# Kernel optimization log

Hardware: AMD Instinct MI355X
Metric: run time of the kernel (lower is better)

## Reference

```python
import jax, jax.numpy as jnp
import numpy as np

B, S, D_IN, D_OUT = 4, 4096, 512, 512


def setup_inputs() -> dict:
    key = jax.random.key(0)
    k1, k2, k3, k4 = jax.random.split(key, 4)
    sc = 1.0 / np.sqrt(D_IN)
    return {
        "x": jax.random.normal(k1, (B, S, D_IN), dtype=jnp.float32),
        "Wq": jax.random.normal(k2, (D_OUT, D_IN), dtype=jnp.float32) * sc,
        "Wk": jax.random.normal(k3, (D_OUT, D_IN), dtype=jnp.float32) * sc,
        "Wv": jax.random.normal(k4, (D_OUT, D_IN), dtype=jnp.float32) * sc,
    }


def reference(x, Wq, Wk, Wv):
    # nn.Linear: y = x @ W.T  (no bias)
    q = jnp.einsum("bsd,ed->bse", x, Wq)  # [B,S,D_OUT]
    k = jnp.einsum("bsd,ed->bse", x, Wk)
    v = jnp.einsum("bsd,ed->bse", x, Wv)
    scale = 1.0 / jnp.sqrt(jnp.asarray(k.shape[-1], dtype=x.dtype))
    scores = jnp.einsum("bqe,bke->bqk", q, k) * scale  # [B,S,S]
    # causal mask: position q attends to k <= q
    s = x.shape[1]
    causal = jnp.tril(jnp.ones((s, s), dtype=bool))
    scores = jnp.where(causal[None, :, :], scores, -jnp.inf)
    attn = jax.nn.softmax(scores, axis=-1)
    # dropout p=0.0 -> identity
    return jnp.einsum("bqk,bke->bqe", attn, v)  # [B,S,D_OUT]
```

## Files before the change

### kernel.cpp

```cpp
#include <hip/hip_runtime.h>

typedef __attribute__((ext_vector_type(8))) short short8;
typedef __attribute__((ext_vector_type(4))) float f32x4;

#define GLD_AS1 const __attribute__((address_space(1))) void*
#define GLD_AS3 __attribute__((address_space(3))) void*

__device__ __forceinline__ unsigned short f2bf(float f) {
  unsigned u = __builtin_bit_cast(unsigned, f);
  u += 0x7fffu + ((u >> 16) & 1u);
  return (unsigned short)(u >> 16);
}
__device__ __forceinline__ float bf2f(unsigned short h) {
  return __builtin_bit_cast(float, (unsigned)h << 16);
}

__global__ void cvt_f32_bf16(const float* __restrict__ in, unsigned short* __restrict__ out, int n4) {
  int i = blockIdx.x * blockDim.x + threadIdx.x;
  const int st = gridDim.x * blockDim.x;
  for (; i < n4; i += st) {
    float4 f = reinterpret_cast<const float4*>(in)[i];
    unsigned long long p = (unsigned long long)f2bf(f.x)
        | ((unsigned long long)f2bf(f.y) << 16)
        | ((unsigned long long)f2bf(f.z) << 32)
        | ((unsigned long long)f2bf(f.w) << 48);
    reinterpret_cast<unsigned long long*>(out)[i] = p;
  }
}

__global__ __launch_bounds__(256) void qkv_gemm(
    const unsigned short* __restrict__ xb, const unsigned short* __restrict__ wcat,
    unsigned short* __restrict__ qb, unsigned short* __restrict__ kb,
    unsigned short* __restrict__ vtb) {
  __shared__ unsigned short As[128 * 64];
  __shared__ unsigned short Bs[128 * 64];
  const int tid = threadIdx.x, lane = tid & 63, w = tid >> 6;
  const int m0 = blockIdx.x * 128, n0 = blockIdx.y * 128;
  const int wr = w >> 1, wc = w & 1;

  f32x4 acc[4][4];
  const f32x4 z4 = {0.f, 0.f, 0.f, 0.f};
  #pragma unroll
  for (int a = 0; a < 4; ++a)
    #pragma unroll
    for (int c = 0; c < 4; ++c) acc[a][c] = z4;

  for (int it = 0; it < 8; ++it) {
    const int k0 = it * 64;
    #pragma unroll
    for (int c = 0; c < 4; ++c) {
      const int rbase = 32 * w + 8 * c;
      const int r = rbase + (lane >> 3);
      const int c16 = (lane & 7) ^ (r & 7);
      const unsigned short* ga = xb + (size_t)(m0 + r) * 512 + k0 + c16 * 8;
      const unsigned short* gb = wcat + (size_t)(n0 + r) * 512 + k0 + c16 * 8;
      __builtin_amdgcn_global_load_lds((GLD_AS1)ga, (GLD_AS3)&As[rbase * 64], 16, 0, 0);
      __builtin_amdgcn_global_load_lds((GLD_AS1)gb, (GLD_AS3)&Bs[rbase * 64], 16, 0, 0);
    }
    __syncthreads();
    #pragma unroll
    for (int ks = 0; ks < 2; ++ks) {
      const int ck = ks * 4 + (lane >> 4);
      short8 av[4], bv[4];
      #pragma unroll
      for (int fr = 0; fr < 4; ++fr) {
        const int rl = 64 * wr + 16 * fr + (lane & 15);
        av[fr] = *reinterpret_cast<const short8*>(&As[rl * 64 + ((ck ^ (rl & 7)) << 3)]);
      }
      #pragma unroll
      for (int fc = 0; fc < 4; ++fc) {
        const int rl = 64 * wc + 16 * fc + (lane & 15);
        bv[fc] = *reinterpret_cast<const short8*>(&Bs[rl * 64 + ((ck ^ (rl & 7)) << 3)]);
      }
      #pragma unroll
      for (int fr = 0; fr < 4; ++fr)
        #pragma unroll
        for (int fc = 0; fc < 4; ++fc)
          acc[fr][fc] = __builtin_amdgcn_mfma_f32_16x16x32_bf16(av[fr], bv[fc], acc[fr][fc], 0, 0, 0);
    }
    __syncthreads();
  }

  const int which = n0 >> 9;
  #pragma unroll
  for (int fr = 0; fr < 4; ++fr) {
    #pragma unroll
    for (int fc = 0; fc < 4; ++fc) {
      const int n = n0 + 64 * wc + 16 * fc + (lane & 15);
      const int nl = n & 511;
      #pragma unroll
      for (int j = 0; j < 4; ++j) {
        const int m = m0 + 64 * wr + 16 * fr + (lane >> 4) * 4 + j;
        const unsigned short v = f2bf(acc[fr][fc][j]);
        if (which == 0)      qb[(size_t)m * 512 + nl] = v;
        else if (which == 1) kb[(size_t)m * 512 + nl] = v;
        else                 vtb[((size_t)((m >> 12) * 512 + nl)) * 4096 + (m & 4095)] = v;
      }
    }
  }
}

__global__ __launch_bounds__(512) void attn_fwd(
    const unsigned short* __restrict__ qg, const unsigned short* __restrict__ kg,
    const unsigned short* __restrict__ vtg,
    float* __restrict__ out0,
    unsigned short* __restrict__ out1,
    float* __restrict__ ml) {
  __shared__ unsigned short Ks[2][64 * 512];
  __shared__ float S_lds[64][66];
  __shared__ unsigned short P_lds[64][72];
  __shared__ float row_f[64];

  const int tid = threadIdx.x, lane = tid & 63, w = tid >> 6;
  const int idx = blockIdx.x;
  const int qt = 63 - (idx >> 3);
  const int b = (idx >> 1) & 3;
  const int half = idx & 1;
  const int nkt = qt + 1;
  const int kt0 = half ? (nkt >> 1) : 0;
  const int kt1 = half ? nkt : (nkt >> 1);
  const int q0 = qt * 64;

  const unsigned short* Qb  = qg  + (size_t)b * 4096 * 512;
  const unsigned short* Kb  = kg  + (size_t)b * 4096 * 512;
  const unsigned short* Vtb = vtg + (size_t)b * 512 * 4096;

  const int wr = w & 3, wc = w >> 2;
  const int dw = w * 64;
  const int srow = 8 * w + (lane >> 3);
  const float scale = 0.044194173824159216f;

  short8 qreg[16];
  {
    const unsigned short* qrow = Qb + (size_t)(q0 + 16 * wr + (lane & 15)) * 512 + (lane >> 4) * 8;
    #pragma unroll
    for (int ks = 0; ks < 16; ++ks)
      qreg[ks] = *reinterpret_cast<const short8*>(qrow + ks * 32);
  }

  const f32x4 z4 = {0.f, 0.f, 0.f, 0.f};
  f32x4 oacc[4][4];
  #pragma unroll
  for (int fr = 0; fr < 4; ++fr)
    #pragma unroll
    for (int fc = 0; fc < 4; ++fc) oacc[fr][fc] = z4;

  float m_run = -1e30f, l_run = 0.f;

  if (kt0 < kt1) {
    #pragma unroll
    for (int r8 = 0; r8 < 8; ++r8) {
      const int r = r8 * 8 + w;
      const unsigned short* g = Kb + (size_t)(kt0 * 64 + r) * 512 + (lane ^ (r & 7)) * 8;
      __builtin_amdgcn_global_load_lds((GLD_AS1)g, (GLD_AS3)&Ks[0][r * 512], 16, 0, 0);
    }
  }
  __syncthreads();

  int cur = 0;
  for (int kt = kt0; kt < kt1; ++kt, cur ^= 1) {
    const int kv0 = kt * 64;

    short8 vreg[2][4];
    #pragma unroll
    for (int ks = 0; ks < 2; ++ks)
      #pragma unroll
      for (int fc = 0; fc < 4; ++fc)
        vreg[ks][fc] = *reinterpret_cast<const short8*>(
            Vtb + (size_t)(dw + 16 * fc + (lane & 15)) * 4096 + kv0 + ks * 32 + (lane >> 4) * 8);

    if (kt + 1 < kt1) {
      #pragma unroll
      for (int r8 = 0; r8 < 8; ++r8) {
        const int r = r8 * 8 + w;
        const unsigned short* g = Kb + (size_t)((kt + 1) * 64 + r) * 512 + (lane ^ (r & 7)) * 8;
        __builtin_amdgcn_global_load_lds((GLD_AS1)g, (GLD_AS3)&Ks[cur ^ 1][r * 512], 16, 0, 0);
      }
    }

    f32x4 sacc[2] = {z4, z4};
    #pragma unroll
    for (int ks = 0; ks < 16; ++ks) {
      const int ck = ks * 4 + (lane >> 4);
      #pragma unroll
      for (int fc = 0; fc < 2; ++fc) {
        const int rl = 32 * wc + 16 * fc + (lane & 15);
        const short8 bv = *reinterpret_cast<const short8*>(&Ks[cur][rl * 512 + ((ck ^ (rl & 7)) << 3)]);
        sacc[fc] = __builtin_amdgcn_mfma_f32_16x16x32_bf16(qreg[ks], bv, sacc[fc], 0, 0, 0);
      }
    }
    #pragma unroll
    for (int fc = 0; fc < 2; ++fc)
      #pragma unroll
      for (int j = 0; j < 4; ++j)
        S_lds[16 * wr + (lane >> 4) * 4 + j][32 * wc + 16 * fc + (lane & 15)] = sacc[fc][j];
    __syncthreads();

    {
      const int c0 = (lane & 7) * 8;
      float v[8];
      #pragma unroll
      for (int i = 0; i < 8; ++i) {
        float s = S_lds[srow][c0 + i] * scale;
        if (kt == qt && (c0 + i) > srow) s = -1e30f;
        v[i] = s;
      }
      float pmax = v[0];
      #pragma unroll
      for (int i = 1; i < 8; ++i) pmax = fmaxf(pmax, v[i]);
      pmax = fmaxf(pmax, __shfl_xor(pmax, 1));
      pmax = fmaxf(pmax, __shfl_xor(pmax, 2));
      pmax = fmaxf(pmax, __shfl_xor(pmax, 4));
      const float m_new = fmaxf(m_run, pmax);
      const float r = __expf(m_run - m_new);
      float psum = 0.f;
      short8 pk;
      #pragma unroll
      for (int i = 0; i < 8; ++i) {
        const float p = __expf(v[i] - m_new);
        psum += p;
        pk[i] = (short)f2bf(p);
      }
      psum += __shfl_xor(psum, 1);
      psum += __shfl_xor(psum, 2);
      psum += __shfl_xor(psum, 4);
      l_run = l_run * r + psum;
      m_run = m_new;
      if ((lane & 7) == 0) row_f[srow] = r;
      *reinterpret_cast<short8*>(&P_lds[srow][c0]) = pk;
    }
    __syncthreads();

    #pragma unroll
    for (int fr = 0; fr < 4; ++fr)
      #pragma unroll
      for (int j = 0; j < 4; ++j) {
        const float f = row_f[16 * fr + (lane >> 4) * 4 + j];
        #pragma unroll
        for (int fc = 0; fc < 4; ++fc) oacc[fr][fc][j] *= f;
      }
    #pragma unroll
    for (int ks = 0; ks < 2; ++ks) {
      short8 av[4];
      #pragma unroll
      for (int fr = 0; fr < 4; ++fr)
        av[fr] = *reinterpret_cast<const short8*>(&P_lds[16 * fr + (lane & 15)][ks * 32 + (lane >> 4) * 8]);
      #pragma unroll
      for (int fr = 0; fr < 4; ++fr)
        #pragma unroll
        for (int fc = 0; fc < 4; ++fc)
          oacc[fr][fc] = __builtin_amdgcn_mfma_f32_16x16x32_bf16(av[fr], vreg[ks][fc], oacc[fr][fc], 0, 0, 0);
    }
  }

  if ((lane & 7) == 0) {
    const int rg = b * 4096 + q0 + srow;
    ml[(half * 2) * 16384 + rg]     = m_run;
    ml[(half * 2 + 1) * 16384 + rg] = l_run;
  }
  if (half == 0) {
    float* ob = out0 + (size_t)b * 4096 * 512;
    #pragma unroll
    for (int fr = 0; fr < 4; ++fr)
      #pragma unroll
      for (int j = 0; j < 4; ++j) {
        const int row = 16 * fr + (lane >> 4) * 4 + j;
        #pragma unroll
        for (int fc = 0; fc < 4; ++fc)
          ob[(size_t)(q0 + row) * 512 + dw + 16 * fc + (lane & 15)] = oacc[fr][fc][j];
      }
  } else {
    unsigned short* ob = out1 + (size_t)b * 4096 * 512;
    #pragma unroll
    for (int fr = 0; fr < 4; ++fr)
      #pragma unroll
      for (int j = 0; j < 4; ++j) {
        const int row = 16 * fr + (lane >> 4) * 4 + j;
        #pragma unroll
        for (int fc = 0; fc < 4; ++fc)
          ob[(size_t)(q0 + row) * 512 + dw + 16 * fc + (lane & 15)] = f2bf(oacc[fr][fc][j]);
      }
  }
}

__global__ void attn_merge(float* __restrict__ out, const unsigned short* __restrict__ o1,
                           const float* __restrict__ ml) {
  const int total = 16384 * 128;
  int i = blockIdx.x * blockDim.x + threadIdx.x;
  const int st = gridDim.x * blockDim.x;
  for (; i < total; i += st) {
    const int r = i >> 7;
    const float m0 = ml[r], l0 = ml[16384 + r];
    const float m1 = ml[2 * 16384 + r], l1 = ml[3 * 16384 + r];
    const float m = fmaxf(m0, m1);
    const float a0 = __expf(m0 - m), a1 = __expf(m1 - m);
    const float inv = 1.0f / (a0 * l0 + a1 * l1);
    const float s0 = a0 * inv, s1 = a1 * inv;
    float4 v0 = reinterpret_cast<const float4*>(out)[i];
    ushort4 v1 = reinterpret_cast<const ushort4*>(o1)[i];
    float4 o;
    o.x = v0.x * s0 + bf2f(v1.x) * s1;
    o.y = v0.y * s0 + bf2f(v1.y) * s1;
    o.z = v0.z * s0 + bf2f(v1.z) * s1;
    o.w = v0.w * s0 + bf2f(v1.w) * s1;
    reinterpret_cast<float4*>(out)[i] = o;
  }
}

extern "C" void kernel_launch(void* const* d_in, const int* in_sizes, int n_in,
                              void* d_out, int out_size, void* d_ws, size_t ws_size,
                              hipStream_t stream) {
  const float* x  = (const float*)d_in[0];
  const float* wq = (const float*)d_in[1];
  const float* wk = (const float*)d_in[2];
  const float* wv = (const float*)d_in[3];

  char* ws = (char*)d_ws;
  unsigned short* xb   = (unsigned short*)(ws);
  unsigned short* wcat = (unsigned short*)(ws + (16u << 20));
  float*          mlp  = (float*)(ws + (18u << 20));
  unsigned short* qb   = (unsigned short*)(ws + (20u << 20));
  unsigned short* kb   = (unsigned short*)(ws + (36u << 20));
  unsigned short* vtb  = (unsigned short*)(ws + (52u << 20));

  cvt_f32_bf16<<<2048, 256, 0, stream>>>(x, xb, (4 * 4096 * 512) / 4);
  cvt_f32_bf16<<<256, 256, 0, stream>>>(wq, wcat, (512 * 512) / 4);
  cvt_f32_bf16<<<256, 256, 0, stream>>>(wk, wcat + 512 * 512, (512 * 512) / 4);
  cvt_f32_bf16<<<256, 256, 0, stream>>>(wv, wcat + 2 * 512 * 512, (512 * 512) / 4);

  qkv_gemm<<<dim3(128, 12), 256, 0, stream>>>(xb, wcat, qb, kb, vtb);

  attn_fwd<<<512, 512, 0, stream>>>(qb, kb, vtb, (float*)d_out, xb, mlp);
  attn_merge<<<2048, 256, 0, stream>>>((float*)d_out, xb, mlp);
}
```

Before: 225.2 us.

## Pipeline QK of next tile with softmax/PV and compute softmax in registers

Folds the softmax scale and log2(e) into Q during the QKV GEMM so the attention kernel can use exp2 directly. Softmax now runs on the MFMA accumulator layout in registers, with only per-row max and sum partials exchanged through LDS, instead of staging the full S tile through shared memory. The K tile is prefetched two steps ahead, and the next tile's QK^T runs while the current P·V is pending, using s_setprio around the MFMA blocks. A launch bound of two blocks per CU is requested, which constrains register usage and risks spills given the large register-resident Q, O and S state.

```diff
diff --git a/kernel.cpp b/kernel.cpp
--- a/kernel.cpp
+++ b/kernel.cpp
@@ -37,6 +37,7 @@
   const int tid = threadIdx.x, lane = tid & 63, w = tid >> 6;
   const int m0 = blockIdx.x * 128, n0 = blockIdx.y * 128;
   const int wr = w >> 1, wc = w & 1;
+  const float QSCALE = 0.0637587085f;
 
   f32x4 acc[4][4];
   const f32x4 z4 = {0.f, 0.f, 0.f, 0.f};
@@ -91,7 +92,8 @@
       #pragma unroll
       for (int j = 0; j < 4; ++j) {
         const int m = m0 + 64 * wr + 16 * fr + (lane >> 4) * 4 + j;
-        const unsigned short v = f2bf(acc[fr][fc][j]);
+        const float a = acc[fr][fc][j];
+        const unsigned short v = f2bf(which == 0 ? a * QSCALE : a);
         if (which == 0)      qb[(size_t)m * 512 + nl] = v;
         else if (which == 1) kb[(size_t)m * 512 + nl] = v;
         else                 vtb[((size_t)((m >> 12) * 512 + nl)) * 4096 + (m & 4095)] = v;
@@ -100,16 +102,17 @@
   }
 }
 
-__global__ __launch_bounds__(512) void attn_fwd(
+__global__ __launch_bounds__(512, 2) void attn_fwd(
     const unsigned short* __restrict__ qg, const unsigned short* __restrict__ kg,
     const unsigned short* __restrict__ vtg,
     float* __restrict__ out0,
     unsigned short* __restrict__ out1,
     float* __restrict__ ml) {
-  __shared__ unsigned short Ks[2][64 * 512];
-  __shared__ float S_lds[64][66];
-  __shared__ unsigned short P_lds[64][72];
-  __shared__ float row_f[64];
+  __shared__ __align__(16) unsigned short Ks[2][64 * 512];
+  __shared__ __align__(16) unsigned short P_lds[64][72];
+  __shared__ __align__(16) float pmx[2][64];
+  __shared__ __align__(16) float psums[2][64];
+  __shared__ __align__(16) float rowr[64];
 
   const int tid = threadIdx.x, lane = tid & 63, w = tid >> 6;
   const int idx = blockIdx.x;
@@ -125,10 +128,8 @@
   const unsigned short* Kb  = kg  + (size_t)b * 4096 * 512;
   const unsigned short* Vtb = vtg + (size_t)b * 512 * 4096;
 
-  const int wr = w & 3, wc = w >> 2;
-  const int dw = w * 64;
-  const int srow = 8 * w + (lane >> 3);
-  const float scale = 0.044194173824159216f;
+  const int wr = w & 3, wc = w >> 2, g = lane >> 4, dw = w * 64;
+  const int rbase = 16 * wr + 4 * g;
 
   short8 qreg[16];
   {
@@ -145,118 +146,167 @@
     #pragma unroll
     for (int fc = 0; fc < 4; ++fc) oacc[fr][fc] = z4;
 
-  float m_run = -1e30f, l_run = 0.f;
+  float m_run[4], l_run[4], rr[4];
+  #pragma unroll
+  for (int j = 0; j < 4; ++j) { m_run[j] = -1e30f; l_run[j] = 0.f; rr[j] = 1.f; }
+
+  short8 vreg[2][4];
+  f32x4 sacc_cur[2], sacc_nxt[2];
+
+#define STAGE_K(kt_, buf_) do {                                                          \
+    _Pragma("unroll")                                                                    \
+    for (int r8 = 0; r8 < 8; ++r8) {                                                     \
+      const int r_ = r8 * 8 + w;                                                         \
+      const unsigned short* g_ = Kb + (size_t)((kt_) * 64 + r_) * 512 + (lane ^ (r_ & 7)) * 8; \
+      __builtin_amdgcn_global_load_lds((GLD_AS1)g_, (GLD_AS3)&Ks[buf_][r_ * 512], 16, 0, 0);   \
+    }                                                                                    \
+  } while (0)
+
+#define QK_TILE(buf_, S_) do {                                                           \
+    _Pragma("unroll")                                                                    \
+    for (int ks = 0; ks < 16; ++ks) {                                                    \
+      const int ck = ks * 4 + (lane >> 4);                                               \
+      _Pragma("unroll")                                                                  \
+      for (int fc = 0; fc < 2; ++fc) {                                                   \
+        const int rl = 32 * wc + 16 * fc + (lane & 15);                                  \
+        const short8 bv = *reinterpret_cast<const short8*>(                              \
+            &Ks[buf_][rl * 512 + ((ck ^ (rl & 7)) << 3)]);                               \
+        S_[fc] = __builtin_amdgcn_mfma_f32_16x16x32_bf16(qreg[ks], bv, S_[fc], 0, 0, 0); \
+      }                                                                                  \
+    }                                                                                    \
+  } while (0)
+
+#define PV_STEP() do {                                                                   \
+    const f32x4 s0 = *reinterpret_cast<const f32x4*>(&psums[0][rbase]);                  \
+    const f32x4 s1 = *reinterpret_cast<const f32x4*>(&psums[1][rbase]);                  \
+    _Pragma("unroll")                                                                    \
+    for (int j = 0; j < 4; ++j) l_run[j] = l_run[j] * rr[j] + s0[j] + s1[j];             \
+    _Pragma("unroll")                                                                    \
+    for (int fr = 0; fr < 4; ++fr) {                                                     \
+      const f32x4 rf = *reinterpret_cast<const f32x4*>(&rowr[16 * fr + 4 * g]);          \
+      _Pragma("unroll")                                                                  \
+      for (int fc = 0; fc < 4; ++fc)                                                     \
+        _Pragma("unroll")                                                                \
+        for (int j = 0; j < 4; ++j) oacc[fr][fc][j] *= rf[j];                            \
+    }                                                                                    \
+    _Pragma("unroll")                                                                    \
+    for (int ks = 0; ks < 2; ++ks) {                                                     \
+      short8 av[4];                                                                      \
+      _Pragma("unroll")                                                                  \
+      for (int fr = 0; fr < 4; ++fr)                                                     \
+        av[fr] = *reinterpret_cast<const short8*>(                                       \
+            &P_lds[16 * fr + (lane & 15)][ks * 32 + (lane >> 4) * 8]);                   \
+      __builtin_amdgcn_s_setprio(1);                                                     \
+      _Pragma("unroll")                                                                  \
+      for (int fr = 0; fr < 4; ++fr)                                                     \
+        _Pragma("unroll")                                                                \
+        for (int fc = 0; fc < 4; ++fc)                                                   \
+          oacc[fr][fc] = __builtin_amdgcn_mfma_f32_16x16x32_bf16(av[fr], vreg[ks][fc],   \
+                                                                 oacc[fr][fc], 0, 0, 0);\
+      __builtin_amdgcn_s_setprio(0);                                                     \
+    }                                                                                    \
+  } while (0)
 
   if (kt0 < kt1) {
-    #pragma unroll
-    for (int r8 = 0; r8 < 8; ++r8) {
-      const int r = r8 * 8 + w;
-      const unsigned short* g = Kb + (size_t)(kt0 * 64 + r) * 512 + (lane ^ (r & 7)) * 8;
-      __builtin_amdgcn_global_load_lds((GLD_AS1)g, (GLD_AS3)&Ks[0][r * 512], 16, 0, 0);
+    STAGE_K(kt0, 0);
+    if (kt0 + 1 < kt1) STAGE_K(kt0 + 1, 1);
+    __syncthreads();
+    sacc_cur[0] = z4; sacc_cur[1] = z4;
+    QK_TILE(0, sacc_cur);
+    __syncthreads();
+
+    int cur = 0;
+    for (int t = kt0; t < kt1; ++t, cur ^= 1) {
+      if (t + 2 < kt1) STAGE_K(t + 2, cur);
+      if (t > kt0) PV_STEP();
+      if (t == qt) {
+        #pragma unroll
+        for (int fc = 0; fc < 2; ++fc) {
+          const int col = 32 * wc + 16 * fc + (lane & 15);
+          #pragma unroll
+          for (int j = 0; j < 4; ++j)
+            if (col > rbase + j) sacc_cur[fc][j] = -1e30f;
+        }
+      }
+      {
+        float pm[4];
+        #pragma unroll
+        for (int j = 0; j < 4; ++j) pm[j] = fmaxf(sacc_cur[0][j], sacc_cur[1][j]);
+        #pragma unroll
+        for (int j = 0; j < 4; ++j) {
+          pm[j] = fmaxf(pm[j], __shfl_xor(pm[j], 1));
+          pm[j] = fmaxf(pm[j], __shfl_xor(pm[j], 2));
+          pm[j] = fmaxf(pm[j], __shfl_xor(pm[j], 4));
+          pm[j] = fmaxf(pm[j], __shfl_xor(pm[j], 8));
+        }
+        if ((lane & 15) == 0) {
+          f32x4 t4 = {pm[0], pm[1], pm[2], pm[3]};
+          *reinterpret_cast<f32x4*>(&pmx[wc][rbase]) = t4;
+        }
+      }
+      __syncthreads();
+
+      const int kv0 = t * 64;
+      #pragma unroll
+      for (int ks = 0; ks < 2; ++ks)
+        #pragma unroll
+        for (int fc = 0; fc < 4; ++fc)
+          vreg[ks][fc] = *reinterpret_cast<const short8*>(
+              Vtb + (size_t)(dw + 16 * fc + (lane & 15)) * 4096 + kv0 + ks * 32 + (lane >> 4) * 8);
+      {
+        const f32x4 pa = *reinterpret_cast<const f32x4*>(&pmx[0][rbase]);
+        const f32x4 pb = *reinterpret_cast<const f32x4*>(&pmx[1][rbase]);
+        float p0[4], p1[4], ps[4];
+        #pragma unroll
+        for (int j = 0; j < 4; ++j) {
+          const float mt = fmaxf(pa[j], pb[j]);
+          const float mn = fmaxf(m_run[j], mt);
+          rr[j] = __builtin_amdgcn_exp2f(m_run[j] - mn);
+          m_run[j] = mn;
+          p0[j] = __builtin_amdgcn_exp2f(sacc_cur[0][j] - mn);
+          p1[j] = __builtin_amdgcn_exp2f(sacc_cur[1][j] - mn);
+          ps[j] = p0[j] + p1[j];
+        }
+        #pragma unroll
+        for (int j = 0; j < 4; ++j) {
+          ps[j] += __shfl_xor(ps[j], 1);
+          ps[j] += __shfl_xor(ps[j], 2);
+          ps[j] += __shfl_xor(ps[j], 4);
+          ps[j] += __shfl_xor(ps[j], 8);
+        }
+        if ((lane & 15) == 0) {
+          f32x4 t4 = {ps[0], ps[1], ps[2], ps[3]};
+          *reinterpret_cast<f32x4*>(&psums[wc][rbase]) = t4;
+          if (wc == 0) {
+            f32x4 r4 = {rr[0], rr[1], rr[2], rr[3]};
+            *reinterpret_cast<f32x4*>(&rowr[rbase]) = r4;
+          }
+        }
+        const int colb = 32 * wc + (lane & 15);
+        #pragma unroll
+        for (int j = 0; j < 4; ++j) {
+          P_lds[rbase + j][colb]      = f2bf(p0[j]);
+          P_lds[rbase + j][colb + 16] = f2bf(p1[j]);
+        }
+      }
+      if (t + 1 < kt1) {
+        sacc_nxt[0] = z4; sacc_nxt[1] = z4;
+        __builtin_amdgcn_s_setprio(1);
+        QK_TILE(cur ^ 1, sacc_nxt);
+        __builtin_amdgcn_s_setprio(0);
+        sacc_cur[0] = sacc_nxt[0]; sacc_cur[1] = sacc_nxt[1];
+      }
+      __syncthreads();
     }
-  }
-  __syncthreads();
-
-  int cur = 0;
-  for (int kt = kt0; kt < kt1; ++kt, cur ^= 1) {
-    const int kv0 = kt * 64;
-
-    short8 vreg[2][4];
-    #pragma unroll
-    for (int ks = 0; ks < 2; ++ks)
-      #pragma unroll
-      for (int fc = 0; fc < 4; ++fc)
-        vreg[ks][fc] = *reinterpret_cast<const short8*>(
-            Vtb + (size_t)(dw + 16 * fc + (lane & 15)) * 4096 + kv0 + ks * 32 + (lane >> 4) * 8);
-
-    if (kt + 1 < kt1) {
-      #pragma unroll
-      for (int r8 = 0; r8 < 8; ++r8) {
-        const int r = r8 * 8 + w;
-        const unsigned short* g = Kb + (size_t)((kt + 1) * 64 + r) * 512 + (lane ^ (r & 7)) * 8;
-        __builtin_amdgcn_global_load_lds((GLD_AS1)g, (GLD_AS3)&Ks[cur ^ 1][r * 512], 16, 0, 0);
-      }
-    }
-
-    f32x4 sacc[2] = {z4, z4};
-    #pragma unroll
-    for (int ks = 0; ks < 16; ++ks) {
-      const int ck = ks * 4 + (lane >> 4);
-      #pragma unroll
-      for (int fc = 0; fc < 2; ++fc) {
-        const int rl = 32 * wc + 16 * fc + (lane & 15);
-        const short8 bv = *reinterpret_cast<const short8*>(&Ks[cur][rl * 512 + ((ck ^ (rl & 7)) << 3)]);
-        sacc[fc] = __builtin_amdgcn_mfma_f32_16x16x32_bf16(qreg[ks], bv, sacc[fc], 0, 0, 0);
-      }
-    }
-    #pragma unroll
-    for (int fc = 0; fc < 2; ++fc)
-      #pragma unroll
-      for (int j = 0; j < 4; ++j)
-        S_lds[16 * wr + (lane >> 4) * 4 + j][32 * wc + 16 * fc + (lane & 15)] = sacc[fc][j];
-    __syncthreads();
-
-    {
-      const int c0 = (lane & 7) * 8;
-      float v[8];
-      #pragma unroll
-      for (int i = 0; i < 8; ++i) {
-        float s = S_lds[srow][c0 + i] * scale;
-        if (kt == qt && (c0 + i) > srow) s = -1e30f;
-        v[i] = s;
-      }
-      float pmax = v[0];
-      #pragma unroll
-      for (int i = 1; i < 8; ++i) pmax = fmaxf(pmax, v[i]);
-      pmax = fmaxf(pmax, __shfl_xor(pmax, 1));
-      pmax = fmaxf(pmax, __shfl_xor(pmax, 2));
-      pmax = fmaxf(pmax, __shfl_xor(pmax, 4));
-      const float m_new = fmaxf(m_run, pmax);
-      const float r = __expf(m_run - m_new);
-      float psum = 0.f;
-      short8 pk;
-      #pragma unroll
-      for (int i = 0; i < 8; ++i) {
-        const float p = __expf(v[i] - m_new);
-        psum += p;
-        pk[i] = (short)f2bf(p);
-      }
-      psum += __shfl_xor(psum, 1);
-      psum += __shfl_xor(psum, 2);
-      psum += __shfl_xor(psum, 4);
-      l_run = l_run * r + psum;
-      m_run = m_new;
-      if ((lane & 7) == 0) row_f[srow] = r;
-      *reinterpret_cast<short8*>(&P_lds[srow][c0]) = pk;
-    }
-    __syncthreads();
-
-    #pragma unroll
-    for (int fr = 0; fr < 4; ++fr)
-      #pragma unroll
-      for (int j = 0; j < 4; ++j) {
-        const float f = row_f[16 * fr + (lane >> 4) * 4 + j];
-        #pragma unroll
-        for (int fc = 0; fc < 4; ++fc) oacc[fr][fc][j] *= f;
-      }
-    #pragma unroll
-    for (int ks = 0; ks < 2; ++ks) {
-      short8 av[4];
-      #pragma unroll
-      for (int fr = 0; fr < 4; ++fr)
-        av[fr] = *reinterpret_cast<const short8*>(&P_lds[16 * fr + (lane & 15)][ks * 32 + (lane >> 4) * 8]);
-      #pragma unroll
-      for (int fr = 0; fr < 4; ++fr)
-        #pragma unroll
-        for (int fc = 0; fc < 4; ++fc)
-          oacc[fr][fc] = __builtin_amdgcn_mfma_f32_16x16x32_bf16(av[fr], vreg[ks][fc], oacc[fr][fc], 0, 0, 0);
-    }
-  }
-
-  if ((lane & 7) == 0) {
-    const int rg = b * 4096 + q0 + srow;
-    ml[(half * 2) * 16384 + rg]     = m_run;
-    ml[(half * 2 + 1) * 16384 + rg] = l_run;
+    PV_STEP();
+  }
+
+  if ((lane & 15) == 0 && wc == 0) {
+    const int rg = b * 4096 + q0 + rbase;
+    f32x4 m4 = {m_run[0], m_run[1], m_run[2], m_run[3]};
+    f32x4 l4 = {l_run[0], l_run[1], l_run[2], l_run[3]};
+    *reinterpret_cast<f32x4*>(&ml[(half * 2) * 16384 + rg])     = m4;
+    *reinterpret_cast<f32x4*>(&ml[(half * 2 + 1) * 16384 + rg]) = l4;
   }
   if (half == 0) {
     float* ob = out0 + (size_t)b * 4096 * 512;
@@ -281,6 +331,9 @@
           ob[(size_t)(q0 + row) * 512 + dw + 16 * fc + (lane & 15)] = f2bf(oacc[fr][fc][j]);
       }
   }
+#undef STAGE_K
+#undef QK_TILE
+#undef PV_STEP
 }
 
 __global__ void attn_merge(float* __restrict__ out, const unsigned short* __restrict__ o1,
@@ -293,7 +346,7 @@
     const float m0 = ml[r], l0 = ml[16384 + r];
     const float m1 = ml[2 * 16384 + r], l1 = ml[3 * 16384 + r];
     const float m = fmaxf(m0, m1);
-    const float a0 = __expf(m0 - m), a1 = __expf(m1 - m);
+    const float a0 = __builtin_amdgcn_exp2f(m0 - m), a1 = __builtin_amdgcn_exp2f(m1 - m);
     const float inv = 1.0f / (a0 * l0 + a1 * l1);
     const float s0 = a0 * inv, s1 = a1 * inv;
     float4 v0 = reinterpret_cast<const float4*>(out)[i];
```

After: 226.8 us. Within noise of the previous version (+0.7%).
